# Optimization experiments

Hardware: AMD Instinct MI355X
Metric: run time of the kernel (lower is better)

## Reference

```python
import jax, jax.numpy as jnp
import numpy as np

N, E, D_IN, H, L = 50000, 800000, 256, 128, 6


def setup_inputs() -> dict:
    key = jax.random.key(0)
    ks = jax.random.split(key, 16)
    s = 0.05
    return {
        "x": jax.random.normal(ks[0], (N, D_IN), jnp.float32),
        "edge_index": jax.random.randint(ks[1], (2, E), 0, N, jnp.int32),
        "y": jax.random.randint(ks[2], (N,), 0, L, jnp.int32),
        # input projection (stored [in, out])
        "lin_w": jax.random.normal(ks[3], (D_IN, H), jnp.float32) * s,
        "lin_b": jnp.zeros((H,), jnp.float32),
        # GatedGraphConv 1: message weight [H,H], GRUCell params (torch layout [3H,H])
        "w1": jax.random.normal(ks[4], (H, H), jnp.float32) * s,
        "wih1": jax.random.normal(ks[5], (3 * H, H), jnp.float32) * s,
        "whh1": jax.random.normal(ks[6], (3 * H, H), jnp.float32) * s,
        "bih1": jnp.zeros((3 * H,), jnp.float32),
        "bhh1": jnp.zeros((3 * H,), jnp.float32),
        # GatedGraphConv 2
        "w2": jax.random.normal(ks[7], (H, H), jnp.float32) * s,
        "wih2": jax.random.normal(ks[8], (3 * H, H), jnp.float32) * s,
        "whh2": jax.random.normal(ks[9], (3 * H, H), jnp.float32) * s,
        "bih2": jnp.zeros((3 * H,), jnp.float32),
        "bhh2": jnp.zeros((3 * H,), jnp.float32),
        # classifier
        "cls_w": jax.random.normal(ks[10], (H, L), jnp.float32) * s,
        "cls_b": jnp.zeros((L,), jnp.float32),
    }


def _gated_conv(h, src, dst, w, wih, whh, bih, bhh):
    # PyG GatedGraphConv, num_layers=1: m = h @ W; aggregate add src->dst; GRUCell(m_agg, h)
    m = h @ w                                   # [N,H]
    agg = jax.ops.segment_sum(m[src], dst, num_segments=N)  # scatter-add [N,H]
    gi = agg @ wih.T + bih                      # [N,3H]
    gh = h @ whh.T + bhh                        # [N,3H]
    i_r, i_z, i_n = jnp.split(gi, 3, axis=-1)
    h_r, h_z, h_n = jnp.split(gh, 3, axis=-1)
    r = jax.nn.sigmoid(i_r + h_r)
    z = jax.nn.sigmoid(i_z + h_z)
    n = jnp.tanh(i_n + r * h_n)
    return (1.0 - z) * n + z * h


def reference(x, edge_index, y, lin_w, lin_b, w1, wih1, whh1, bih1, bhh1,
              w2, wih2, whh2, bih2, bhh2, cls_w, cls_b):
    src, dst = edge_index[0], edge_index[1]
    h = x @ lin_w + lin_b                       # [N,H]
    h = _gated_conv(h, src, dst, w1, wih1, whh1, bih1, bhh1)
    h = jax.nn.elu(h)
    h = _gated_conv(h, src, dst, w2, wih2, whh2, bih2, bhh2)
    features = h
    output = h @ cls_w + cls_b                  # [N,L]
    logp = jax.nn.log_softmax(output, axis=-1)
    loss = -jnp.mean(jnp.take_along_axis(logp, y[:, None], axis=-1))
    return output, loss, features
```

## Files before the change

### kernel.cpp

```cpp
#include <hip/hip_runtime.h>
#include <cstddef>
#include <cstdint>

typedef __attribute__((ext_vector_type(8))) short bf16x8;
typedef __attribute__((ext_vector_type(4))) float f32x4;
typedef __attribute__((ext_vector_type(8))) unsigned short u16x8;

__device__ inline unsigned short f2bf(float f) {
    unsigned u = __builtin_bit_cast(unsigned, f);
    u += 0x7FFF + ((u >> 16) & 1);
    return (unsigned short)(u >> 16);
}
__device__ inline float bfbits_lo(unsigned v) { return __builtin_bit_cast(float, v << 16); }
__device__ inline float bfbits_hi(unsigned v) { return __builtin_bit_cast(float, v & 0xffff0000u); }
__device__ inline float bf2f(unsigned short b) { return __builtin_bit_cast(float, (unsigned)b << 16); }

__device__ inline float fsigmoid(float x) { return 1.0f / (1.0f + __expf(-x)); }
__device__ inline float ftanh(float x)    { return 1.0f - 2.0f / (__expf(2.0f * x) + 1.0f); }

__device__ inline int swzB(int row, int slot) {
    return row * 64 + ((slot ^ ((row >> 1) & 3)) << 4);
}
__device__ inline bf16x8 ldbf8(const unsigned short* p) {
    u16x8 v = *(const u16x8*)p;
    return __builtin_bit_cast(bf16x8, v);
}

__global__ __launch_bounds__(256)
void prepack_kernel(const float* __restrict__ S, unsigned short* __restrict__ P,
                    int K, int C, int trans)
{
    int idx = blockIdx.x * 256 + threadIdx.x;
    if (idx >= K * C) return;
    int kk = idx & 31;
    int c  = (idx >> 5) % C;
    int kc = idx / (32 * C);
    int k  = kc * 32 + kk;
    float v = trans ? S[(size_t)c * K + k] : S[(size_t)k * C + c];
    P[idx] = f2bf(v);
}

__global__ __launch_bounds__(256)
void wcomb_kernel(const float* __restrict__ Wm, const float* __restrict__ Wih,
                  unsigned short* __restrict__ P)
{
    int idx = blockIdx.x * 256 + threadIdx.x;
    int kk = idx & 31;
    int c  = (idx >> 5) % 384;
    int kc = idx / (32 * 384);
    int d  = kc * 32 + kk;
    const float4* a = (const float4*)&Wm[(size_t)d * 128];
    const float4* b = (const float4*)&Wih[(size_t)c * 128];
    float s = 0.0f;
#pragma unroll 8
    for (int t = 0; t < 32; ++t) {
        float4 av = a[t], bv = b[t];
        s += av.x * bv.x + av.y * bv.y + av.z * bv.z + av.w * bv.w;
    }
    P[idx] = f2bf(s);
}

template<int KC>
__global__ __launch_bounds__(256)
void mfma_xw(const float* __restrict__ A, const unsigned short* __restrict__ P,
             const float* __restrict__ bias, unsigned short* __restrict__ Cbf, int M)
{
    __shared__ unsigned short Ab[KC * 2048];
    const int tid  = threadIdx.x;
    const int l    = tid & 63;
    const int w    = tid >> 6;
    const int wr   = w >> 1, wc = w & 1;
    const int row0 = blockIdx.x * 64;
    const int K    = KC * 32;

    {
        int row = tid >> 2, slot = tid & 3, kpos = slot * 8;
#pragma unroll
        for (int kc = 0; kc < KC; ++kc) {
            unsigned short u[8];
            if (row0 + row < M) {
                const float* src = &A[(size_t)(row0 + row) * K + kc * 32 + kpos];
                float4 v0 = *(const float4*)src;
                float4 v1 = *(const float4*)(src + 4);
                u[0]=f2bf(v0.x); u[1]=f2bf(v0.y); u[2]=f2bf(v0.z); u[3]=f2bf(v0.w);
                u[4]=f2bf(v1.x); u[5]=f2bf(v1.y); u[6]=f2bf(v1.z); u[7]=f2bf(v1.w);
            } else {
#pragma unroll
                for (int q = 0; q < 8; ++q) u[q] = 0;
            }
            *(u16x8*)((char*)Ab + kc * 4096 + swzB(row, slot)) = *(u16x8*)u;
        }
    }
    __syncthreads();

    f32x4 acc[2][4];
#pragma unroll
    for (int i = 0; i < 2; ++i)
#pragma unroll
        for (int j = 0; j < 4; ++j) acc[i][j] = (f32x4){0.f, 0.f, 0.f, 0.f};

#pragma unroll
    for (int kc = 0; kc < KC; ++kc) {
        bf16x8 af[2], bf[4];
#pragma unroll
        for (int rt = 0; rt < 2; ++rt)
            af[rt] = *(const bf16x8*)((const char*)Ab + kc * 4096 +
                                      swzB(wr * 32 + rt * 16 + (l & 15), l >> 4));
#pragma unroll
        for (int ct = 0; ct < 4; ++ct) {
            int c = wc * 64 + ct * 16 + (l & 15);
            bf[ct] = ldbf8(&P[(size_t)kc * 4096 + c * 32 + (l >> 4) * 8]);
        }
#pragma unroll
        for (int rt = 0; rt < 2; ++rt)
#pragma unroll
            for (int ct = 0; ct < 4; ++ct)
                acc[rt][ct] = __builtin_amdgcn_mfma_f32_16x16x32_bf16(af[rt], bf[ct], acc[rt][ct], 0, 0, 0);
    }

#pragma unroll
    for (int rt = 0; rt < 2; ++rt)
#pragma unroll
        for (int ct = 0; ct < 4; ++ct) {
            int col = wc * 64 + ct * 16 + (l & 15);
            float bv = bias ? bias[col] : 0.0f;
#pragma unroll
            for (int j = 0; j < 4; ++j) {
                int row = row0 + wr * 32 + rt * 16 + (l >> 4) * 4 + j;
                if (row < M) Cbf[(size_t)row * 128 + col] = f2bf(acc[rt][ct][j] + bv);
            }
        }
}

template<int ELU, int OUTF32>
__global__ __launch_bounds__(512, 2)
void mfma_gru(const unsigned short* __restrict__ agghbf, const unsigned short* __restrict__ hbf,
              const unsigned short* __restrict__ wcP, const unsigned short* __restrict__ whhP,
              const float* __restrict__ bih, const float* __restrict__ bhh,
              float* __restrict__ hout, unsigned short* __restrict__ houtbf,
              int M, int ntiles)
{
    __shared__ unsigned short Aa[4096];
    __shared__ unsigned short Ah[4096];
    const int tid = threadIdx.x;
    const int l   = tid & 63;
    const int g   = tid >> 6;

    const int skc = tid >> 7;
    const int t3  = tid & 127;
    const int srow = t3 >> 2, sslot = t3 & 3, skpos = sslot * 8;
    const int slbyte = skc * 2048 + swzB(srow, sslot);

    const int unit = g * 16 + (l & 15);
    const int kcu = unit >> 5, slotu = (unit & 31) >> 3, elemu = unit & 7;
    const float bir = bih[unit], biz = bih[128 + unit], bin = bih[256 + unit];
    const float bhr = bhh[unit], bhz = bhh[128 + unit], bhn = bhh[256 + unit];

    bf16x8 BW[4][3], BU[4][3];
#pragma unroll
    for (int kc = 0; kc < 4; ++kc)
#pragma unroll
        for (int gr = 0; gr < 3; ++gr) {
            int c = gr * 128 + g * 16 + (l & 15);
            size_t boff = (size_t)kc * 12288 + c * 32 + (l >> 4) * 8;
            BW[kc][gr] = ldbf8(&wcP[boff]);
            BU[kc][gr] = ldbf8(&whhP[boff]);
        }

    u16x8 ua = (u16x8){0,0,0,0,0,0,0,0};
    u16x8 uh = (u16x8){0,0,0,0,0,0,0,0};
    {
        int row0 = blockIdx.x * 32;
        if (row0 + srow < M && row0 < ntiles * 32) {
            size_t goff = (size_t)(row0 + srow) * 128 + skc * 32 + skpos;
            ua = *(const u16x8*)&agghbf[goff];
            uh = *(const u16x8*)&hbf[goff];
        }
    }

    for (int t = blockIdx.x; t < ntiles; t += gridDim.x) {
        const int row0 = t * 32;
        __syncthreads();
        *(u16x8*)((char*)Aa + slbyte) = ua;
        *(u16x8*)((char*)Ah + slbyte) = uh;
        __syncthreads();

        {
            int tn = t + gridDim.x;
            ua = (u16x8){0,0,0,0,0,0,0,0};
            uh = (u16x8){0,0,0,0,0,0,0,0};
            if (tn < ntiles) {
                int r0n = tn * 32;
                if (r0n + srow < M) {
                    size_t goff = (size_t)(r0n + srow) * 128 + skc * 32 + skpos;
                    ua = *(const u16x8*)&agghbf[goff];
                    uh = *(const u16x8*)&hbf[goff];
                }
            }
        }

        f32x4 gi[3][2], gh[3][2];
#pragma unroll
        for (int gr = 0; gr < 3; ++gr)
#pragma unroll
            for (int rt = 0; rt < 2; ++rt) {
                gi[gr][rt] = (f32x4){0.f, 0.f, 0.f, 0.f};
                gh[gr][rt] = (f32x4){0.f, 0.f, 0.f, 0.f};
            }

#pragma unroll
        for (int kc = 0; kc < 4; ++kc) {
            bf16x8 aa[2], ah[2];
#pragma unroll
            for (int rt = 0; rt < 2; ++rt) {
                int lbyte = kc * 2048 + swzB(rt * 16 + (l & 15), l >> 4);
                aa[rt] = *(const bf16x8*)((const char*)Aa + lbyte);
                ah[rt] = *(const bf16x8*)((const char*)Ah + lbyte);
            }
#pragma unroll
            for (int gr = 0; gr < 3; ++gr)
#pragma unroll
                for (int rt = 0; rt < 2; ++rt) {
                    gi[gr][rt] = __builtin_amdgcn_mfma_f32_16x16x32_bf16(aa[rt], BW[kc][gr], gi[gr][rt], 0, 0, 0);
                    gh[gr][rt] = __builtin_amdgcn_mfma_f32_16x16x32_bf16(ah[rt], BU[kc][gr], gh[gr][rt], 0, 0, 0);
                }
        }

#pragma unroll
        for (int rt = 0; rt < 2; ++rt)
#pragma unroll
            for (int j = 0; j < 4; ++j) {
                int rl = rt * 16 + (l >> 4) * 4 + j;
                int row = row0 + rl;
                if (row >= M) continue;
                float hv = bf2f(*(const unsigned short*)
                                ((const char*)Ah + kcu * 2048 + swzB(rl, slotu) + elemu * 2));
                float rr = fsigmoid(gi[0][rt][j] + bir + gh[0][rt][j] + bhr);
                float z  = fsigmoid(gi[1][rt][j] + biz + gh[1][rt][j] + bhz);
                float nn = ftanh(gi[2][rt][j] + bin + rr * (gh[2][rt][j] + bhn));
                float o  = (1.0f - z) * nn + z * hv;
                if (ELU) o = (o > 0.0f) ? o : (__expf(o) - 1.0f);
                if (OUTF32) hout[(size_t)row * 128 + unit] = o;
                else        houtbf[(size_t)row * 128 + unit] = f2bf(o);
            }
    }
}


#define CHUNK 4096

__global__ __launch_bounds__(1024)
void chunk_hist_kernel(const int* __restrict__ dst, int* __restrict__ bh, int E)
{
    __shared__ int lh[256];
    const int c = blockIdx.x, tid = threadIdx.x;
    if (tid < 256) lh[tid] = 0;
    __syncthreads();
#pragma unroll
    for (int q = 0; q < 4; ++q) {
        int e = c * CHUNK + q * 1024 + tid;
        if (e < E) atomicAdd(&lh[dst[e] >> 8], 1);
    }
    __syncthreads();
    if (tid < 256) bh[c * 256 + tid] = lh[tid];
}

__global__ __launch_bounds__(256)
void colscan_kernel(int* __restrict__ bh, int* __restrict__ bcnt, int NCH)
{
    __shared__ int wt[4];
    __shared__ int carry;
    const int b = blockIdx.x;
    const int tid = threadIdx.x, lane = tid & 63, w4 = tid >> 6;
    if (tid == 0) carry = 0;
    __syncthreads();
    for (int base = 0; base < NCH; base += 256) {
        int c = base + tid;
        int v = (c < NCH) ? bh[c * 256 + b] : 0;
        int s = v;
#pragma unroll
        for (int o = 1; o < 64; o <<= 1) {
            int n = __shfl_up(s, o, 64);
            if (lane >= o) s += n;
        }
        if (lane == 63) wt[w4] = s;
        __syncthreads();
        int wpre = 0;
        for (int q = 0; q < w4; ++q) wpre += wt[q];
        int ex = carry + wpre + s - v;
        if (c < NCH) bh[c * 256 + b] = ex;
        __syncthreads();
        if (tid == 255) carry = ex + v;
        __syncthreads();
    }
    if (tid == 0) bcnt[b] = carry;
}

__global__ __launch_bounds__(256)
void bscan2_kernel(const int* __restrict__ bcnt, int* __restrict__ bbase,
                   int* __restrict__ off, int N, int E)
{
    __shared__ int wt[4];
    const int tid = threadIdx.x, lane = tid & 63, w4 = tid >> 6;
    int v = bcnt[tid];
    int s = v;
#pragma unroll
    for (int o = 1; o < 64; o <<= 1) {
        int n = __shfl_up(s, o, 64);
        if (lane >= o) s += n;
    }
    if (lane == 63) wt[w4] = s;
    __syncthreads();
    int wpre = 0;
    for (int q = 0; q < w4; ++q) wpre += wt[q];
    bbase[tid] = wpre + s - v;
    if (tid == 0) off[N] = E;
}

__global__ __launch_bounds__(1024)
void place_kernel(const int* __restrict__ src, const int* __restrict__ dst,
                  const int* __restrict__ bh, const int* __restrict__ bbase,
                  unsigned long long* __restrict__ bpair, int E)
{
    __shared__ int cur[256];
    const int c = blockIdx.x, tid = threadIdx.x;
    if (tid < 256) cur[tid] = bbase[tid] + bh[c * 256 + tid];
    __syncthreads();
#pragma unroll
    for (int q = 0; q < 4; ++q) {
        int e = c * CHUNK + q * 1024 + tid;
        if (e < E) {
            int d = dst[e];
            int pos = atomicAdd(&cur[d >> 8], 1);
            bpair[(size_t)pos] = ((unsigned long long)(unsigned)d << 32) | (unsigned)src[e];
        }
    }
}

__global__ __launch_bounds__(1024)
void bucket_sort_kernel(const unsigned long long* __restrict__ bpair,
                        const int* __restrict__ bcnt, const int* __restrict__ bbase,
                        int* __restrict__ off, int* __restrict__ ssrc, int N)
{
    __shared__ int hist[256];
    __shared__ int wt[4];
    const int b = blockIdx.x;
    const int tid = threadIdx.x;
    const int cnt = bcnt[b];
    const int base = bbase[b];

    if (tid < 256) hist[tid] = 0;
    __syncthreads();
    for (int i = tid; i < cnt; i += 1024) {
        unsigned long long p = bpair[(size_t)base + i];
        atomicAdd(&hist[(int)(p >> 32) & 255], 1);
    }
    __syncthreads();

    int ex = 0;
    {
        int lane = tid & 63, w4 = tid >> 6;
        int v = (tid < 256) ? hist[tid] : 0;
        int s = v;
#pragma unroll
        for (int o = 1; o < 64; o <<= 1) {
            int n = __shfl_up(s, o, 64);
            if (lane >= o) s += n;
        }
        if (tid < 256 && lane == 63) wt[w4] = s;
        __syncthreads();
        if (tid < 256) {
            int wpre = 0;
            for (int q = 0; q < w4; ++q) wpre += wt[q];
            ex = wpre + s - v;
        }
    }
    __syncthreads();
    if (tid < 256) {
        int d = (b << 8) + tid;
        if (d < N) off[d] = base + ex;
        hist[tid] = ex;
    }
    __syncthreads();
    for (int i = tid; i < cnt; i += 1024) {
        unsigned long long p = bpair[(size_t)base + i];
        int d = (int)(p >> 32) & 255;
        int pos = atomicAdd(&hist[d], 1);
        ssrc[(size_t)base + pos] = (int)(unsigned)p;
    }
}

__global__ __launch_bounds__(256)
void gather_agg_bf(const unsigned short* __restrict__ m, const int* __restrict__ off,
                   const int* __restrict__ ssrc, unsigned short* __restrict__ agg, int N)
{
    int w = (blockIdx.x * 256 + threadIdx.x) >> 6;
    int lane = threadIdx.x & 63;
    if (w >= N) return;
    int half = lane >> 5, hl = lane & 31;
    int e0 = off[w], e1 = off[w + 1];
    float a0[4] = {0.f, 0.f, 0.f, 0.f};
    float a1[4] = {0.f, 0.f, 0.f, 0.f};
    int e = e0 + half;
    for (; e + 2 < e1; e += 4) {
        int s0 = ssrc[e], s1 = ssrc[e + 2];
        uint2 v0 = *(const uint2*)&m[(size_t)s0 * 128 + hl * 4];
        uint2 v1 = *(const uint2*)&m[(size_t)s1 * 128 + hl * 4];
        a0[0] += bfbits_lo(v0.x); a0[1] += bfbits_hi(v0.x);
        a0[2] += bfbits_lo(v0.y); a0[3] += bfbits_hi(v0.y);
        a1[0] += bfbits_lo(v1.x); a1[1] += bfbits_hi(v1.x);
        a1[2] += bfbits_lo(v1.y); a1[3] += bfbits_hi(v1.y);
    }
    if (e < e1) {
        int s0 = ssrc[e];
        uint2 v0 = *(const uint2*)&m[(size_t)s0 * 128 + hl * 4];
        a0[0] += bfbits_lo(v0.x); a0[1] += bfbits_hi(v0.x);
        a0[2] += bfbits_lo(v0.y); a0[3] += bfbits_hi(v0.y);
    }
    float o[4];
#pragma unroll
    for (int j = 0; j < 4; ++j) o[j] = a0[j] + a1[j];
#pragma unroll
    for (int j = 0; j < 4; ++j) o[j] += __shfl_xor(o[j], 32, 64);
    if (half == 0) {
        uint2 pk;
        pk.x = (unsigned)f2bf(o[0]) | ((unsigned)f2bf(o[1]) << 16);
        pk.y = (unsigned)f2bf(o[2]) | ((unsigned)f2bf(o[3]) << 16);
        *(uint2*)&agg[(size_t)w * 128 + hl * 4] = pk;
    }
}

__global__ __launch_bounds__(256)
void cls_kernel(const float* __restrict__ h, const float* __restrict__ W,
                const float* __restrict__ b, const int* __restrict__ y,
                float* __restrict__ logitsOut, float* __restrict__ partials,
                int N, float invN)
{
    __shared__ float pl[4];
    const int wid  = threadIdx.x >> 6;
    const int lane = threadIdx.x & 63;
    const int gw   = blockIdx.x * 4 + wid;
    if (threadIdx.x < 4) pl[threadIdx.x] = 0.0f;
    __syncthreads();
    if (gw < N) {
        float h0 = h[(size_t)gw * 128 + lane * 2];
        float h1 = h[(size_t)gw * 128 + lane * 2 + 1];
        float acc[6];
#pragma unroll
        for (int c = 0; c < 6; ++c)
            acc[c] = h0 * W[(lane * 2) * 6 + c] + h1 * W[(lane * 2 + 1) * 6 + c];
#pragma unroll
        for (int off = 32; off >= 1; off >>= 1)
#pragma unroll
            for (int c = 0; c < 6; ++c)
                acc[c] += __shfl_xor(acc[c], off, 64);
        float logit[6];
#pragma unroll
        for (int c = 0; c < 6; ++c) logit[c] = acc[c] + b[c];
#pragma unroll
        for (int c = 0; c < 6; ++c)
            if (lane == c) logitsOut[(size_t)gw * 6 + c] = logit[c];
        if (lane == 0) {
            float mx = logit[0];
#pragma unroll
            for (int c = 1; c < 6; ++c) mx = fmaxf(mx, logit[c]);
            float se = 0.0f;
#pragma unroll
            for (int c = 0; c < 6; ++c) se += expf(logit[c] - mx);
            float lse = mx + logf(se);
            int yy = y[gw];
            float ly = 0.0f;
#pragma unroll
            for (int c = 0; c < 6; ++c)
                if (yy == c) ly = logit[c];
            pl[wid] = (lse - ly) * invN;
        }
    }
    __syncthreads();
    if (threadIdx.x == 0)
        partials[blockIdx.x] = pl[0] + pl[1] + pl[2] + pl[3];
}

__global__ __launch_bounds__(1024)
void loss_reduce(const float* __restrict__ partials, float* __restrict__ loss, int P)
{
    __shared__ float buf[1024];
    float s = 0.0f;
    for (int i = threadIdx.x; i < (unsigned)P; i += 1024) s += partials[i];
    buf[threadIdx.x] = s;
    __syncthreads();
    for (int o = 512; o >= 1; o >>= 1) {
        if (threadIdx.x < (unsigned)o) buf[threadIdx.x] += buf[threadIdx.x + o];
        __syncthreads();
    }
    if (threadIdx.x == 0) loss[0] = buf[0];
}

extern "C" void kernel_launch(void* const* d_in, const int* in_sizes, int n_in,
                              void* d_out, int out_size, void* d_ws, size_t ws_size,
                              hipStream_t stream)
{
    const float* x     = (const float*)d_in[0];
    const int*   eidx  = (const int*)d_in[1];
    const int*   y     = (const int*)d_in[2];
    const float* lin_w = (const float*)d_in[3];
    const float* lin_b = (const float*)d_in[4];
    const float* w1    = (const float*)d_in[5];
    const float* wih1  = (const float*)d_in[6];
    const float* whh1  = (const float*)d_in[7];
    const float* bih1  = (const float*)d_in[8];
    const float* bhh1  = (const float*)d_in[9];
    const float* w2    = (const float*)d_in[10];
    const float* wih2  = (const float*)d_in[11];
    const float* whh2  = (const float*)d_in[12];
    const float* bih2  = (const float*)d_in[13];
    const float* bhh2  = (const float*)d_in[14];
    const float* cls_w = (const float*)d_in[15];
    const float* cls_b = (const float*)d_in[16];

    const int N   = in_sizes[2];
    const int E   = in_sizes[1] / 2;
    const int L   = 6;
    const size_t NH = (size_t)N * 128;
    const int P   = (N + 3) / 4;
    const int NT  = (N + 31) / 32;
    const int NCH = (E + CHUNK - 1) / CHUNK;
    const int NBK = (N + 255) >> 8;

    float* out    = (float*)d_out;
    float* logits = out;
    float* loss   = out + (size_t)N * L;
    float* feats  = out + (size_t)N * L + 1;

    float* ws   = (float*)d_ws;
    float* part = ws;

    unsigned short* h_bf   = (unsigned short*)(part + P);
    unsigned short* aggh   = h_bf + NH;
    unsigned short* linP   = aggh + NH;
    unsigned short* wc1P   = linP  + 32768;
    unsigned short* whh1P  = wc1P  + 49152;
    unsigned short* wc2P   = whh1P + 49152;
    unsigned short* whh2P  = wc2P  + 49152;

    int* off   = (int*)(whh2P + 49152);
    int* bcnt  = off + (N + 2);
    int* bbase = bcnt + 256;
    int* bh    = bbase + 256;
    unsigned long long* bpair =
        (unsigned long long*)(((uintptr_t)(bh + (size_t)NCH * 256) + 7) & ~(uintptr_t)7);
    int* ssrc  = (int*)(bpair + E);

    const int* src = eidx;
    const int* dst = eidx + E;

    dim3 blk(256);
    unsigned ngridW = (unsigned)((N + 3) / 4);
    unsigned gemmG  = (unsigned)((N + 63) / 64);
    unsigned gruG   = (unsigned)(NT < 256 ? NT : 256);

    chunk_hist_kernel<<<dim3((unsigned)NCH), dim3(1024), 0, stream>>>(dst, bh, E);
    colscan_kernel<<<dim3(256), dim3(256), 0, stream>>>(bh, bcnt, NCH);
    bscan2_kernel<<<dim3(1), dim3(256), 0, stream>>>(bcnt, bbase, off, N, E);
    place_kernel<<<dim3((unsigned)NCH), dim3(1024), 0, stream>>>(src, dst, bh, bbase, bpair, E);
    bucket_sort_kernel<<<dim3((unsigned)NBK), dim3(1024), 0, stream>>>(bpair, bcnt, bbase, off, ssrc, N);

    prepack_kernel<<<dim3(128), blk, 0, stream>>>(lin_w, linP, 256, 128, 0);
    wcomb_kernel<<<dim3(192), blk, 0, stream>>>(w1, wih1, wc1P);
    wcomb_kernel<<<dim3(192), blk, 0, stream>>>(w2, wih2, wc2P);
    prepack_kernel<<<dim3(192), blk, 0, stream>>>(whh1, whh1P, 128, 384, 1);
    prepack_kernel<<<dim3(192), blk, 0, stream>>>(whh2, whh2P, 128, 384, 1);

    mfma_xw<8><<<dim3(gemmG), blk, 0, stream>>>(x, linP, lin_b, h_bf, N);

    gather_agg_bf<<<dim3(ngridW), blk, 0, stream>>>(h_bf, off, ssrc, aggh, N);
    mfma_gru<1, 0><<<dim3(gruG), dim3(512), 0, stream>>>(aggh, h_bf, wc1P, whh1P, bih1, bhh1, nullptr, h_bf, N, NT);

    gather_agg_bf<<<dim3(ngridW), blk, 0, stream>>>(h_bf, off, ssrc, aggh, N);
    mfma_gru<0, 1><<<dim3(gruG), dim3(512), 0, stream>>>(aggh, h_bf, wc2P, whh2P, bih2, bhh2, feats, nullptr, N, NT);

    cls_kernel<<<dim3(ngridW), blk, 0, stream>>>(feats, cls_w, cls_b, y, logits, part, N, 1.0f / (float)N);
    loss_reduce<<<dim3(1), dim3(1024), 0, stream>>>(part, loss, P);
}
```

Before: 228.9 us.

## Fuse neighbor gather-aggregation into GRU MFMA kernel, one tile per block

Removes the separate gather_agg_bf kernel and makes each GRU block gather and sum the neighbor rows for its 32-row tile directly into shared memory before the MFMA GEMMs. This drops the global write and re-read of the aggregated buffer and two kernel launches. The persistent grid-stride loop with register prefetch is replaced by one tile per block, and ping-pong h buffers are used because other blocks still read the input h. Each thread now walks its row's full edge list serially with 16-byte loads, which may expose gather latency and load imbalance from degree skew.

```diff
diff --git a/kernel.cpp b/kernel.cpp
--- a/kernel.cpp
+++ b/kernel.cpp
@@ -134,11 +134,11 @@
 
 template<int ELU, int OUTF32>
 __global__ __launch_bounds__(512, 2)
-void mfma_gru(const unsigned short* __restrict__ agghbf, const unsigned short* __restrict__ hbf,
+void mfma_gru(const int* __restrict__ off, const int* __restrict__ ssrc,
+              const unsigned short* __restrict__ hbf,
               const unsigned short* __restrict__ wcP, const unsigned short* __restrict__ whhP,
               const float* __restrict__ bih, const float* __restrict__ bhh,
-              float* __restrict__ hout, unsigned short* __restrict__ houtbf,
-              int M, int ntiles)
+              float* __restrict__ hout, unsigned short* __restrict__ houtbf, int M)
 {
     __shared__ unsigned short Aa[4096];
     __shared__ unsigned short Ah[4096];
@@ -150,6 +150,7 @@
     const int t3  = tid & 127;
     const int srow = t3 >> 2, sslot = t3 & 3, skpos = sslot * 8;
     const int slbyte = skc * 2048 + swzB(srow, sslot);
+    const int row0 = blockIdx.x * 32;
 
     const int unit = g * 16 + (l & 15);
     const int kcu = unit >> 5, slotu = (unit & 31) >> 3, elemu = unit & 7;
@@ -167,83 +168,92 @@
             BU[kc][gr] = ldbf8(&whhP[boff]);
         }
 
-    u16x8 ua = (u16x8){0,0,0,0,0,0,0,0};
-    u16x8 uh = (u16x8){0,0,0,0,0,0,0,0};
     {
-        int row0 = blockIdx.x * 32;
-        if (row0 + srow < M && row0 < ntiles * 32) {
-            size_t goff = (size_t)(row0 + srow) * 128 + skc * 32 + skpos;
-            ua = *(const u16x8*)&agghbf[goff];
+        int row = row0 + srow;
+        u16x8 uh = (u16x8){0,0,0,0,0,0,0,0};
+        float g0[4] = {0.f, 0.f, 0.f, 0.f};
+        float g1[4] = {0.f, 0.f, 0.f, 0.f};
+        if (row < M) {
+            size_t goff = (size_t)row * 128 + skc * 32 + skpos;
             uh = *(const u16x8*)&hbf[goff];
-        }
-    }
-
-    for (int t = blockIdx.x; t < ntiles; t += gridDim.x) {
-        const int row0 = t * 32;
-        __syncthreads();
+            int e0 = off[row], e1 = off[row + 1];
+            int e = e0;
+            for (; e + 1 < e1; e += 2) {
+                int s0 = ssrc[e], s1 = ssrc[e + 1];
+                uint4 v0 = *(const uint4*)&hbf[(size_t)s0 * 128 + skc * 32 + skpos];
+                uint4 v1 = *(const uint4*)&hbf[(size_t)s1 * 128 + skc * 32 + skpos];
+                g0[0] += bfbits_lo(v0.x); g0[1] += bfbits_hi(v0.x);
+                g0[2] += bfbits_lo(v0.y); g0[3] += bfbits_hi(v0.y);
+                g1[0] += bfbits_lo(v0.z); g1[1] += bfbits_hi(v0.z);
+                g1[2] += bfbits_lo(v0.w); g1[3] += bfbits_hi(v0.w);
+                g0[0] += bfbits_lo(v1.x); g0[1] += bfbits_hi(v1.x);
+                g0[2] += bfbits_lo(v1.y); g0[3] += bfbits_hi(v1.y);
+                g1[0] += bfbits_lo(v1.z); g1[1] += bfbits_hi(v1.z);
+                g1[2] += bfbits_lo(v1.w); g1[3] += bfbits_hi(v1.w);
+            }
+            if (e < e1) {
+                int s0 = ssrc[e];
+                uint4 v0 = *(const uint4*)&hbf[(size_t)s0 * 128 + skc * 32 + skpos];
+                g0[0] += bfbits_lo(v0.x); g0[1] += bfbits_hi(v0.x);
+                g0[2] += bfbits_lo(v0.y); g0[3] += bfbits_hi(v0.y);
+                g1[0] += bfbits_lo(v0.z); g1[1] += bfbits_hi(v0.z);
+                g1[2] += bfbits_lo(v0.w); g1[3] += bfbits_hi(v0.w);
+            }
+        }
+        u16x8 ua;
+        ua[0] = f2bf(g0[0]); ua[1] = f2bf(g0[1]);
+        ua[2] = f2bf(g0[2]); ua[3] = f2bf(g0[3]);
+        ua[4] = f2bf(g1[0]); ua[5] = f2bf(g1[1]);
+        ua[6] = f2bf(g1[2]); ua[7] = f2bf(g1[3]);
         *(u16x8*)((char*)Aa + slbyte) = ua;
         *(u16x8*)((char*)Ah + slbyte) = uh;
-        __syncthreads();
-
-        {
-            int tn = t + gridDim.x;
-            ua = (u16x8){0,0,0,0,0,0,0,0};
-            uh = (u16x8){0,0,0,0,0,0,0,0};
-            if (tn < ntiles) {
-                int r0n = tn * 32;
-                if (r0n + srow < M) {
-                    size_t goff = (size_t)(r0n + srow) * 128 + skc * 32 + skpos;
-                    ua = *(const u16x8*)&agghbf[goff];
-                    uh = *(const u16x8*)&hbf[goff];
-                }
+    }
+    __syncthreads();
+
+    f32x4 gi[3][2], gh[3][2];
+#pragma unroll
+    for (int gr = 0; gr < 3; ++gr)
+#pragma unroll
+        for (int rt = 0; rt < 2; ++rt) {
+            gi[gr][rt] = (f32x4){0.f, 0.f, 0.f, 0.f};
+            gh[gr][rt] = (f32x4){0.f, 0.f, 0.f, 0.f};
+        }
+
+#pragma unroll
+    for (int kc = 0; kc < 4; ++kc) {
+        bf16x8 aa[2], ah[2];
+#pragma unroll
+        for (int rt = 0; rt < 2; ++rt) {
+            int lbyte = kc * 2048 + swzB(rt * 16 + (l & 15), l >> 4);
+            aa[rt] = *(const bf16x8*)((const char*)Aa + lbyte);
+            ah[rt] = *(const bf16x8*)((const char*)Ah + lbyte);
+        }
+#pragma unroll
+        for (int gr = 0; gr < 3; ++gr)
+#pragma unroll
+            for (int rt = 0; rt < 2; ++rt) {
+                gi[gr][rt] = __builtin_amdgcn_mfma_f32_16x16x32_bf16(aa[rt], BW[kc][gr], gi[gr][rt], 0, 0, 0);
+                gh[gr][rt] = __builtin_amdgcn_mfma_f32_16x16x32_bf16(ah[rt], BU[kc][gr], gh[gr][rt], 0, 0, 0);
             }
-        }
-
-        f32x4 gi[3][2], gh[3][2];
-#pragma unroll
-        for (int gr = 0; gr < 3; ++gr)
-#pragma unroll
-            for (int rt = 0; rt < 2; ++rt) {
-                gi[gr][rt] = (f32x4){0.f, 0.f, 0.f, 0.f};
-                gh[gr][rt] = (f32x4){0.f, 0.f, 0.f, 0.f};
-            }
-
-#pragma unroll
-        for (int kc = 0; kc < 4; ++kc) {
-            bf16x8 aa[2], ah[2];
-#pragma unroll
-            for (int rt = 0; rt < 2; ++rt) {
-                int lbyte = kc * 2048 + swzB(rt * 16 + (l & 15), l >> 4);
-                aa[rt] = *(const bf16x8*)((const char*)Aa + lbyte);
-                ah[rt] = *(const bf16x8*)((const char*)Ah + lbyte);
-            }
-#pragma unroll
-            for (int gr = 0; gr < 3; ++gr)
-#pragma unroll
-                for (int rt = 0; rt < 2; ++rt) {
-                    gi[gr][rt] = __builtin_amdgcn_mfma_f32_16x16x32_bf16(aa[rt], BW[kc][gr], gi[gr][rt], 0, 0, 0);
-                    gh[gr][rt] = __builtin_amdgcn_mfma_f32_16x16x32_bf16(ah[rt], BU[kc][gr], gh[gr][rt], 0, 0, 0);
-                }
-        }
-
-#pragma unroll
-        for (int rt = 0; rt < 2; ++rt)
-#pragma unroll
-            for (int j = 0; j < 4; ++j) {
-                int rl = rt * 16 + (l >> 4) * 4 + j;
-                int row = row0 + rl;
-                if (row >= M) continue;
-                float hv = bf2f(*(const unsigned short*)
-                                ((const char*)Ah + kcu * 2048 + swzB(rl, slotu) + elemu * 2));
-                float rr = fsigmoid(gi[0][rt][j] + bir + gh[0][rt][j] + bhr);
-                float z  = fsigmoid(gi[1][rt][j] + biz + gh[1][rt][j] + bhz);
-                float nn = ftanh(gi[2][rt][j] + bin + rr * (gh[2][rt][j] + bhn));
-                float o  = (1.0f - z) * nn + z * hv;
-                if (ELU) o = (o > 0.0f) ? o : (__expf(o) - 1.0f);
-                if (OUTF32) hout[(size_t)row * 128 + unit] = o;
-                else        houtbf[(size_t)row * 128 + unit] = f2bf(o);
-            }
-    }
+    }
+
+#pragma unroll
+    for (int rt = 0; rt < 2; ++rt)
+#pragma unroll
+        for (int j = 0; j < 4; ++j) {
+            int rl = rt * 16 + (l >> 4) * 4 + j;
+            int row = row0 + rl;
+            if (row >= M) continue;
+            float hv = bf2f(*(const unsigned short*)
+                            ((const char*)Ah + kcu * 2048 + swzB(rl, slotu) + elemu * 2));
+            float rr = fsigmoid(gi[0][rt][j] + bir + gh[0][rt][j] + bhr);
+            float z  = fsigmoid(gi[1][rt][j] + biz + gh[1][rt][j] + bhz);
+            float nn = ftanh(gi[2][rt][j] + bin + rr * (gh[2][rt][j] + bhn));
+            float o  = (1.0f - z) * nn + z * hv;
+            if (ELU) o = (o > 0.0f) ? o : (__expf(o) - 1.0f);
+            if (OUTF32) hout[(size_t)row * 128 + unit] = o;
+            else        houtbf[(size_t)row * 128 + unit] = f2bf(o);
+        }
 }
 
 
@@ -387,46 +397,6 @@
         int d = (int)(p >> 32) & 255;
         int pos = atomicAdd(&hist[d], 1);
         ssrc[(size_t)base + pos] = (int)(unsigned)p;
-    }
-}
-
-__global__ __launch_bounds__(256)
-void gather_agg_bf(const unsigned short* __restrict__ m, const int* __restrict__ off,
-                   const int* __restrict__ ssrc, unsigned short* __restrict__ agg, int N)
-{
-    int w = (blockIdx.x * 256 + threadIdx.x) >> 6;
-    int lane = threadIdx.x & 63;
-    if (w >= N) return;
-    int half = lane >> 5, hl = lane & 31;
-    int e0 = off[w], e1 = off[w + 1];
-    float a0[4] = {0.f, 0.f, 0.f, 0.f};
-    float a1[4] = {0.f, 0.f, 0.f, 0.f};
-    int e = e0 + half;
-    for (; e + 2 < e1; e += 4) {
-        int s0 = ssrc[e], s1 = ssrc[e + 2];
-        uint2 v0 = *(const uint2*)&m[(size_t)s0 * 128 + hl * 4];
-        uint2 v1 = *(const uint2*)&m[(size_t)s1 * 128 + hl * 4];
-        a0[0] += bfbits_lo(v0.x); a0[1] += bfbits_hi(v0.x);
-        a0[2] += bfbits_lo(v0.y); a0[3] += bfbits_hi(v0.y);
-        a1[0] += bfbits_lo(v1.x); a1[1] += bfbits_hi(v1.x);
-        a1[2] += bfbits_lo(v1.y); a1[3] += bfbits_hi(v1.y);
-    }
-    if (e < e1) {
-        int s0 = ssrc[e];
-        uint2 v0 = *(const uint2*)&m[(size_t)s0 * 128 + hl * 4];
-        a0[0] += bfbits_lo(v0.x); a0[1] += bfbits_hi(v0.x);
-        a0[2] += bfbits_lo(v0.y); a0[3] += bfbits_hi(v0.y);
-    }
-    float o[4];
-#pragma unroll
-    for (int j = 0; j < 4; ++j) o[j] = a0[j] + a1[j];
-#pragma unroll
-    for (int j = 0; j < 4; ++j) o[j] += __shfl_xor(o[j], 32, 64);
-    if (half == 0) {
-        uint2 pk;
-        pk.x = (unsigned)f2bf(o[0]) | ((unsigned)f2bf(o[1]) << 16);
-        pk.y = (unsigned)f2bf(o[2]) | ((unsigned)f2bf(o[3]) << 16);
-        *(uint2*)&agg[(size_t)w * 128 + hl * 4] = pk;
     }
 }
 
@@ -536,8 +506,8 @@
     float* part = ws;
 
     unsigned short* h_bf   = (unsigned short*)(part + P);
-    unsigned short* aggh   = h_bf + NH;
-    unsigned short* linP   = aggh + NH;
+    unsigned short* hb2    = h_bf + NH;
+    unsigned short* linP   = hb2 + NH;
     unsigned short* wc1P   = linP  + 32768;
     unsigned short* whh1P  = wc1P  + 49152;
     unsigned short* wc2P   = whh1P + 49152;
@@ -557,7 +527,6 @@
     dim3 blk(256);
     unsigned ngridW = (unsigned)((N + 3) / 4);
     unsigned gemmG  = (unsigned)((N + 63) / 64);
-    unsigned gruG   = (unsigned)(NT < 256 ? NT : 256);
 
     chunk_hist_kernel<<<dim3((unsigned)NCH), dim3(1024), 0, stream>>>(dst, bh, E);
     colscan_kernel<<<dim3(256), dim3(256), 0, stream>>>(bh, bcnt, NCH);
@@ -573,11 +542,9 @@
 
     mfma_xw<8><<<dim3(gemmG), blk, 0, stream>>>(x, linP, lin_b, h_bf, N);
 
-    gather_agg_bf<<<dim3(ngridW), blk, 0, stream>>>(h_bf, off, ssrc, aggh, N);
-    mfma_gru<1, 0><<<dim3(gruG), dim3(512), 0, stream>>>(aggh, h_bf, wc1P, whh1P, bih1, bhh1, nullptr, h_bf, N, NT);
-
-    gather_agg_bf<<<dim3(ngridW), blk, 0, stream>>>(h_bf, off, ssrc, aggh, N);
-    mfma_gru<0, 1><<<dim3(gruG), dim3(512), 0, stream>>>(aggh, h_bf, wc2P, whh2P, bih2, bhh2, feats, nullptr, N, NT);
+    mfma_gru<1, 0><<<dim3((unsigned)NT), dim3(512), 0, stream>>>(off, ssrc, h_bf, wc1P, whh1P, bih1, bhh1, nullptr, hb2, N);
+
+    mfma_gru<0, 1><<<dim3((unsigned)NT), dim3(512), 0, stream>>>(off, ssrc, hb2, wc2P, whh2P, bih2, bhh2, feats, nullptr, N);
 
     cls_kernel<<<dim3(ngridW), blk, 0, stream>>>(feats, cls_w, cls_b, y, logits, part, N, 1.0f / (float)N);
     loss_reduce<<<dim3(1), dim3(1024), 0, stream>>>(part, loss, P);
```

New measurement: 306.4 us. 1.34x slower.
